# Kernel tuning notes

Measured on AMD Instinct MI355X. Metric: run time of the kernel, lower is better.

## Reference

```python
import jax, jax.numpy as jnp
import numpy as np

T, B, E, H, V, K = 512, 64, 256, 512, 50000, 50
START, STOP = 0, K - 1  # tags = ['<START>'] + tags + ['<STOP>']


def setup_inputs() -> dict:
    key = jax.random.key(0)
    ks = jax.random.split(key, 13)
    p = lambda k, shape, s=0.02: jax.random.normal(k, shape, jnp.float32) * s
    return {
        'tokens': jax.random.randint(ks[0], (T, B), 0, V, dtype=jnp.int32),
        'embed': p(ks[1], (V, E), 0.1),
        'w_ih_f': p(ks[2], (4 * H, E)), 'w_hh_f': p(ks[3], (4 * H, H)), 'b_f': jnp.zeros((4 * H,), jnp.float32),
        'w_ih_b': p(ks[4], (4 * H, E)), 'w_hh_b': p(ks[5], (4 * H, H)), 'b_b': jnp.zeros((4 * H,), jnp.float32),
        'w_enc': p(ks[6], (H, 2 * H)), 'b_enc': jnp.zeros((H,), jnp.float32),
        'w_out': p(ks[7], (K, H)), 'b_out': jnp.zeros((K,), jnp.float32),
        'trans': p(ks[8], (K, K), 0.1),
    }


def _lstm_dir(x, w_ih, w_hh, b, reverse):
    # x: [T,B,E] -> hidden states [T,B,H]; torch gate order i,f,g,o
    bsz = x.shape[1]
    h_dim = w_hh.shape[1]
    xp = jnp.einsum('tbe,ge->tbg', x, w_ih) + b  # precompute input projections

    def step(carry, xt):
        h, c = carry
        g = xt + h @ w_hh.T
        i, f, gg, o = jnp.split(g, 4, axis=-1)
        c = jax.nn.sigmoid(f) * c + jax.nn.sigmoid(i) * jnp.tanh(gg)
        h = jax.nn.sigmoid(o) * jnp.tanh(c)
        return (h, c), h

    init = (jnp.zeros((bsz, h_dim), x.dtype), jnp.zeros((bsz, h_dim), x.dtype))
    _, hs = jax.lax.scan(step, init, xp, reverse=reverse)
    return hs


def reference(tokens, embed, w_ih_f, w_hh_f, b_f, w_ih_b, w_hh_b, b_b,
              w_enc, b_enc, w_out, b_out, trans):
    x = embed[tokens]  # [T,B,E]
    hf = _lstm_dir(x, w_ih_f, w_hh_f, b_f, reverse=False)
    hb = _lstm_dir(x, w_ih_b, w_hh_b, b_b, reverse=True)
    enc = jnp.concatenate([hf, hb], axis=-1)                      # [T,B,2H]
    states = jnp.tanh(jnp.einsum('tbd,hd->tbh', enc, w_enc) + b_enc)
    emit = jnp.einsum('tbh,kh->tbk', states, w_out) + b_out       # [T,B,K]

    # CRF forward algorithm (log partition). trans[j, i] = score of i -> j.
    NEG = jnp.float32(-10000.0)
    bsz, k = emit.shape[1], emit.shape[2]
    alpha0 = jnp.full((bsz, k), NEG).at[:, START].set(0.0)

    def crf_step(alpha, e_t):
        # scores[b, j, i] = alpha[b, i] + trans[j, i] + emit[b, t, j]
        s = alpha[:, None, :] + trans[None, :, :] + e_t[:, :, None]
        return jax.nn.logsumexp(s, axis=-1), None

    alpha, _ = jax.lax.scan(crf_step, alpha0, emit)
    log_z = jax.nn.logsumexp(alpha + trans[STOP][None, :], axis=-1)  # [B]
    return log_z
```

## Files before the change

kernel.cpp:

```cpp
#include <hip/hip_runtime.h>
#include <stdint.h>

#define T_ 512
#define B_ 64
#define E_ 256
#define H_ 512
#define KT 50

typedef __attribute__((ext_vector_type(8))) short bf16x8;
typedef __attribute__((ext_vector_type(4))) float f32x4;
typedef __attribute__((ext_vector_type(4))) int i32x4;

#define MFMA16(a,b,c) __builtin_amdgcn_mfma_f32_16x16x32_bf16((a),(b),(c),0,0,0)

static __device__ __forceinline__ float bf2f(unsigned short v) {
  unsigned int u = ((unsigned int)v) << 16; float f; __builtin_memcpy(&f, &u, 4); return f;
}
static __device__ __forceinline__ unsigned short f2bf(float f) {
  unsigned int u; __builtin_memcpy(&u, &f, 4);
  u += 0x7fffu + ((u >> 16) & 1u);
  return (unsigned short)(u >> 16);
}
static __device__ __forceinline__ float sigm(float x) { return 1.f / (1.f + __expf(-x)); }
static __device__ __forceinline__ float tanh_(float x) { return 2.f / (1.f + __expf(-2.f * x)) - 1.f; }

static __device__ __forceinline__ unsigned int load_dw_dev(const unsigned int* p) {
  unsigned int v;
  asm volatile("global_load_dword %0, %1, off sc0 sc1\n\ts_waitcnt vmcnt(0)"
               : "=v"(v) : "v"(p) : "memory");
  return v;
}

__global__ void probe_kernel(const unsigned short* __restrict__ e,
                             unsigned int* __restrict__ flag) {
  int lane = threadIdx.x & 63;
  float a = fabsf(bf2f(e[2 * lane]));
  int good = (a >= 1e-8f && a <= 4.0f);
  unsigned long long m = __ballot(good);
  if (threadIdx.x == 0) flag[0] = (__popcll(m) >= 48) ? 1u : 0u;
}

struct CvtArgs { const void* src; unsigned short* dst; int n; };
struct CvtPack { CvtArgs a[11]; };

__global__ __launch_bounds__(256) void convert_kernel(CvtPack p,
                                                      const unsigned int* __restrict__ flag) {
  CvtArgs c = p.a[blockIdx.y];
  int i = (blockIdx.x * 256 + threadIdx.x) * 8;
  if (i >= c.n) return;
  int isbf = *flag;
  if (i + 8 <= c.n) {
    if (isbf) {
      *(i32x4*)(c.dst + i) = *(const i32x4*)((const unsigned short*)c.src + i);
    } else {
      const float* s = (const float*)c.src;
      float4 a0 = *(const float4*)(s + i);
      float4 a1 = *(const float4*)(s + i + 4);
      unsigned short o[8] = {f2bf(a0.x), f2bf(a0.y), f2bf(a0.z), f2bf(a0.w),
                             f2bf(a1.x), f2bf(a1.y), f2bf(a1.z), f2bf(a1.w)};
      *(i32x4*)(c.dst + i) = *(i32x4*)o;
    }
  } else {
    for (int j = 0; j < 8; j++) {
      if (i + j < c.n) {
        c.dst[i + j] = isbf ? ((const unsigned short*)c.src)[i + j]
                            : f2bf(((const float*)c.src)[i + j]);
      }
    }
  }
}

__global__ __launch_bounds__(256) void embed_kernel(
    const int* __restrict__ tokens, const void* __restrict__ embed,
    const unsigned int* __restrict__ flag, unsigned short* __restrict__ x) {
  int tid = threadIdx.x;
  int row = blockIdx.x * 8 + (tid >> 5);
  int l = tid & 31;
  int tok = tokens[row];
  if (*flag) {
    const unsigned short* e = (const unsigned short*)embed;
    *(i32x4*)(x + (size_t)row * E_ + l * 8) =
        *(const i32x4*)(e + (size_t)tok * E_ + l * 8);
  } else {
    const float* e = (const float*)embed + (size_t)tok * E_ + l * 8;
    float4 a0 = *(const float4*)e;
    float4 a1 = *(const float4*)(e + 4);
    unsigned short o[8] = {f2bf(a0.x), f2bf(a0.y), f2bf(a0.z), f2bf(a0.w),
                           f2bf(a1.x), f2bf(a1.y), f2bf(a1.z), f2bf(a1.w)};
    *(i32x4*)(x + (size_t)row * E_ + l * 8) = *(i32x4*)o;
  }
}

__global__ __launch_bounds__(256, 1) void lstm_kernel(
    const unsigned short* __restrict__ whh_f, const unsigned short* __restrict__ wih_f,
    const unsigned short* __restrict__ bias_f,
    const unsigned short* __restrict__ whh_b, const unsigned short* __restrict__ wih_b,
    const unsigned short* __restrict__ bias_b,
    const unsigned short* __restrict__ x,
    unsigned short* __restrict__ hf, unsigned short* __restrict__ hb,
    unsigned int* __restrict__ tags) {
  const int tid = threadIdx.x;
  const int wv = tid >> 6, lane = tid & 63, q = lane >> 4, l15 = lane & 15;
  const int bid = blockIdx.x;
  const int dir = bid & 1;
  const int wg = bid >> 1;
  const int u0 = wg * 16;

  const unsigned short* whh = dir ? whh_b : whh_f;
  const unsigned short* wih = dir ? wih_b : wih_f;
  const unsigned short* bvec = dir ? bias_b : bias_f;
  unsigned short* hbuf = dir ? hb : hf;
  unsigned int* tbase = tags + (size_t)dir * 512;

  bf16x8 afrag[4][6];
#pragma unroll
  for (int mt = 0; mt < 4; mt++) {
    int row = mt * H_ + u0 + l15;
#pragma unroll
    for (int kl = 0; kl < 6; kl++) {
      const unsigned short* p = (kl < 4)
          ? (whh + (size_t)row * H_ + (wv * 4 + kl) * 32 + q * 8)
          : (wih + (size_t)row * E_ + (wv * 2 + (kl - 4)) * 32 + q * 8);
      afrag[mt][kl] = *(const bf16x8*)p;
    }
  }

  const int eb = tid & 63;
  const int uu = tid >> 6;
  float bg[4][4];
#pragma unroll
  for (int s = 0; s < 4; s++) {
    int u = uu + 4 * s;
#pragma unroll
    for (int g = 0; g < 4; g++) bg[s][g] = bf2f(bvec[g * H_ + u0 + u]);
  }
  float cst[4] = {0.f, 0.f, 0.f, 0.f};

  __shared__ float pacc[4][64][66];
  __shared__ __align__(16) unsigned short h_out[64][16];
  __shared__ unsigned int go_word;
  if (tid == 0) go_word = 0;

  for (int step = 0; step < T_; step++) {
    const int t = dir ? (T_ - 1 - step) : step;
    f32x4 acc[4][4];
#pragma unroll
    for (int mt = 0; mt < 4; mt++)
#pragma unroll
      for (int nt = 0; nt < 4; nt++) acc[mt][nt] = (f32x4){0.f, 0.f, 0.f, 0.f};

    {
      const unsigned short* xb = x + (size_t)t * B_ * E_;
#pragma unroll
      for (int kl = 4; kl < 6; kl++) {
        int ec = wv * 2 + (kl - 4);
#pragma unroll
        for (int nt = 0; nt < 4; nt++) {
          int b = nt * 16 + l15;
          bf16x8 bx = *(const bf16x8*)(xb + (size_t)b * E_ + ec * 32 + q * 8);
#pragma unroll
          for (int mt = 0; mt < 4; mt++)
            acc[mt][nt] = MFMA16(afrag[mt][kl], bx, acc[mt][nt]);
        }
      }
    }

    if (step > 0) {
      if (wv == 1) {
        const unsigned int* tp = tbase + (size_t)(lane & 31) * 16;
        for (;;) {
          unsigned int v = load_dw_dev(tp);
          unsigned long long m = __ballot((lane < 32) ? (v >= (unsigned)step) : 1);
          if (m == ~0ULL) break;
          __builtin_amdgcn_s_sleep(1);
        }
        __hip_atomic_store(&go_word, (unsigned int)step, __ATOMIC_RELAXED,
                           __HIP_MEMORY_SCOPE_WORKGROUP);
      } else {
        while (__hip_atomic_load(&go_word, __ATOMIC_RELAXED,
                                 __HIP_MEMORY_SCOPE_WORKGROUP) < (unsigned int)step)
          __builtin_amdgcn_s_sleep(1);
      }
      asm volatile("" ::: "memory");

      const int tprev = dir ? (t + 1) : (t - 1);
      const unsigned int* hD = (const unsigned int*)hbuf + (size_t)tprev * 16384;

      const unsigned int* a0 = hD + ((wv * 4 + 0) * 4 + q) * 256 + l15 * 4;
      const unsigned int* a1 = hD + ((wv * 4 + 1) * 4 + q) * 256 + l15 * 4;
      const unsigned int* a2 = hD + ((wv * 4 + 2) * 4 + q) * 256 + l15 * 4;
      const unsigned int* a3 = hD + ((wv * 4 + 3) * 4 + q) * 256 + l15 * 4;
      i32x4 h00, h01, h02, h03, h10, h11, h12, h13;
      i32x4 h20, h21, h22, h23, h30, h31, h32, h33;
      asm volatile(
          "global_load_dwordx4 %0, %16, off sc0 sc1\n\t"
          "global_load_dwordx4 %1, %16, off offset:1024 sc0 sc1\n\t"
          "global_load_dwordx4 %2, %16, off offset:2048 sc0 sc1\n\t"
          "global_load_dwordx4 %3, %16, off offset:3072 sc0 sc1\n\t"
          "global_load_dwordx4 %4, %17, off sc0 sc1\n\t"
          "global_load_dwordx4 %5, %17, off offset:1024 sc0 sc1\n\t"
          "global_load_dwordx4 %6, %17, off offset:2048 sc0 sc1\n\t"
          "global_load_dwordx4 %7, %17, off offset:3072 sc0 sc1\n\t"
          "global_load_dwordx4 %8, %18, off sc0 sc1\n\t"
          "global_load_dwordx4 %9, %18, off offset:1024 sc0 sc1\n\t"
          "global_load_dwordx4 %10, %18, off offset:2048 sc0 sc1\n\t"
          "global_load_dwordx4 %11, %18, off offset:3072 sc0 sc1\n\t"
          "global_load_dwordx4 %12, %19, off sc0 sc1\n\t"
          "global_load_dwordx4 %13, %19, off offset:1024 sc0 sc1\n\t"
          "global_load_dwordx4 %14, %19, off offset:2048 sc0 sc1\n\t"
          "global_load_dwordx4 %15, %19, off offset:3072 sc0 sc1\n\t"
          "s_waitcnt vmcnt(0)"
          : "=&v"(h00), "=&v"(h01), "=&v"(h02), "=&v"(h03),
            "=&v"(h10), "=&v"(h11), "=&v"(h12), "=&v"(h13),
            "=&v"(h20), "=&v"(h21), "=&v"(h22), "=&v"(h23),
            "=&v"(h30), "=&v"(h31), "=&v"(h32), "=&v"(h33)
          : "v"(a0), "v"(a1), "v"(a2), "v"(a3)
          : "memory");
      i32x4 hr4[16] = {h00, h01, h02, h03, h10, h11, h12, h13,
                       h20, h21, h22, h23, h30, h31, h32, h33};
#pragma unroll
      for (int kl = 0; kl < 4; kl++) {
#pragma unroll
        for (int nt = 0; nt < 4; nt++) {
          bf16x8 bh;
          __builtin_memcpy(&bh, &hr4[kl * 4 + nt], 16);
#pragma unroll
          for (int mt = 0; mt < 4; mt++)
            acc[mt][nt] = MFMA16(afrag[mt][kl], bh, acc[mt][nt]);
        }
      }
    }

    __syncthreads();
#pragma unroll
    for (int mt = 0; mt < 4; mt++)
#pragma unroll
      for (int nt = 0; nt < 4; nt++)
#pragma unroll
        for (int r = 0; r < 4; r++)
          pacc[wv][mt * 16 + q * 4 + r][nt * 16 + l15] = acc[mt][nt][r];
    __syncthreads();

#pragma unroll
    for (int s = 0; s < 4; s++) {
      int u = uu + 4 * s;
      float gi = bg[s][0], gf = bg[s][1], gg = bg[s][2], og = bg[s][3];
#pragma unroll
      for (int w = 0; w < 4; w++) {
        gi += pacc[w][u][eb];
        gf += pacc[w][16 + u][eb];
        gg += pacc[w][32 + u][eb];
        og += pacc[w][48 + u][eb];
      }
      float cn = sigm(gf) * cst[s] + sigm(gi) * tanh_(gg);
      cst[s] = cn;
      h_out[eb][u] = f2bf(sigm(og) * tanh_(cn));
    }
    __syncthreads();

    if (wv == 0) {
      unsigned int* gp = (unsigned int*)hbuf + (size_t)t * 16384 + wg * 512 + lane * 4;
      i32x4 v0 = *(const i32x4*)&h_out[lane][0];
      i32x4 v1 = *(const i32x4*)&h_out[lane][8];
      asm volatile(
          "global_store_dwordx4 %0, %1, off sc0 sc1\n\t"
          "global_store_dwordx4 %0, %2, off offset:1024 sc0 sc1\n\t"
          "s_waitcnt vmcnt(0)"
          :: "v"(gp), "v"(v0), "v"(v1) : "memory");
      if (lane == 0) {
        unsigned int* tp = tbase + (size_t)wg * 16;
        unsigned int tv = (unsigned int)(step + 1);
        asm volatile("global_store_dword %0, %1, off sc0 sc1"
                     :: "v"(tp), "v"(tv) : "memory");
      }
    }
  }
}

__global__ __launch_bounds__(256) void enc_kernel(
    const unsigned short* __restrict__ hf, const unsigned short* __restrict__ hb,
    const unsigned short* __restrict__ w_enc, const unsigned short* __restrict__ b_enc,
    unsigned short* __restrict__ states) {
  const int tid = threadIdx.x;
  const int bm = blockIdx.x, bn = blockIdx.y;
  const int wv = tid >> 6, lane = tid & 63, q = lane >> 4, l15 = lane & 15;
  const int wm = wv >> 1, wn = wv & 1;

  __shared__ __align__(16) unsigned short a_lds[128][72];
  __shared__ __align__(16) unsigned short b_lds[128][72];
  __shared__ __align__(16) unsigned short st_lds[128][136];

  f32x4 acc[4][4];
#pragma unroll
  for (int mt = 0; mt < 4; mt++)
#pragma unroll
    for (int nt = 0; nt < 4; nt++) acc[mt][nt] = (f32x4){0.f, 0.f, 0.f, 0.f};

  for (int c = 0; c < 16; c++) {
    const unsigned short* asrc = (c < 8) ? hf : hb;
    int kof = (c & 7) * 64;
#pragma unroll
    for (int p = 0; p < 4; p++) {
      int u_ = tid + p * 256;
      int r = u_ >> 3, wu = u_ & 7;
      int grow = bm * 128 + r;
      *(i32x4*)&a_lds[r][wu * 8] =
          *(const i32x4*)((const unsigned int*)asrc + (size_t)(grow >> 6) * 16384 +
                          (size_t)((kof >> 3) + wu) * 256 + (grow & 63) * 4);
      *(i32x4*)&b_lds[r][wu * 8] =
          *(const i32x4*)(w_enc + (size_t)(bn * 128 + r) * 1024 + c * 64 + wu * 8);
    }
    __syncthreads();
#pragma unroll
    for (int kk = 0; kk < 64; kk += 32) {
      bf16x8 af[4], bfr[4];
#pragma unroll
      for (int mt = 0; mt < 4; mt++)
        af[mt] = *(const bf16x8*)&a_lds[wm * 64 + mt * 16 + l15][kk + q * 8];
#pragma unroll
      for (int nt = 0; nt < 4; nt++)
        bfr[nt] = *(const bf16x8*)&b_lds[wn * 64 + nt * 16 + l15][kk + q * 8];
#pragma unroll
      for (int mt = 0; mt < 4; mt++)
#pragma unroll
        for (int nt = 0; nt < 4; nt++) acc[mt][nt] = MFMA16(af[mt], bfr[nt], acc[mt][nt]);
    }
    __syncthreads();
  }

  float be[4];
#pragma unroll
  for (int nt = 0; nt < 4; nt++)
    be[nt] = bf2f(b_enc[bn * 128 + wn * 64 + nt * 16 + l15]);
#pragma unroll
  for (int mt = 0; mt < 4; mt++)
#pragma unroll
    for (int nt = 0; nt < 4; nt++)
#pragma unroll
      for (int r = 0; r < 4; r++) {
        float v = tanh_(acc[mt][nt][r] + be[nt]);
        st_lds[wm * 64 + mt * 16 + q * 4 + r][wn * 64 + nt * 16 + l15] = f2bf(v);
      }
  __syncthreads();
#pragma unroll
  for (int p = 0; p < 8; p++) {
    int u_ = tid + p * 256;
    int r = u_ >> 4, w = u_ & 15;
    *(i32x4*)(states + (size_t)(bm * 128 + r) * H_ + bn * 128 + w * 8) =
        *(const i32x4*)&st_lds[r][w * 8];
  }
}

__global__ __launch_bounds__(256) void emit_kernel(
    const unsigned short* __restrict__ states, const unsigned short* __restrict__ w_out,
    const unsigned short* __restrict__ b_out, float* __restrict__ emit) {
  const int tid = threadIdx.x;
  const int bm = blockIdx.x;
  const int wv = tid >> 6, lane = tid & 63, q = lane >> 4, l15 = lane & 15;
  const int wm = wv >> 1, wn = wv & 1;

  __shared__ __align__(16) unsigned short wo_lds[64][520];
  __shared__ __align__(16) unsigned short a_lds[128][72];

#pragma unroll
  for (int p = 0; p < 16; p++) {
    int u = tid + p * 256;
    int r = u >> 6, wu = u & 63;
    i32x4 v = {0, 0, 0, 0};
    if (r < KT) v = *(const i32x4*)(w_out + (size_t)r * H_ + wu * 8);
    *(i32x4*)&wo_lds[r][wu * 8] = v;
  }

  f32x4 acc[4][2];
#pragma unroll
  for (int mt = 0; mt < 4; mt++)
#pragma unroll
    for (int nt = 0; nt < 2; nt++) acc[mt][nt] = (f32x4){0.f, 0.f, 0.f, 0.f};

  for (int c = 0; c < 8; c++) {
    __syncthreads();
#pragma unroll
    for (int p = 0; p < 4; p++) {
      int u = tid + p * 256;
      int r = u >> 3, wu = u & 7;
      *(i32x4*)&a_lds[r][wu * 8] =
          *(const i32x4*)(states + (size_t)(bm * 128 + r) * H_ + c * 64 + wu * 8);
    }
    __syncthreads();
#pragma unroll
    for (int kk = 0; kk < 64; kk += 32) {
      bf16x8 af[4], bfr[2];
#pragma unroll
      for (int mt = 0; mt < 4; mt++)
        af[mt] = *(const bf16x8*)&a_lds[wm * 64 + mt * 16 + l15][kk + q * 8];
#pragma unroll
      for (int nt = 0; nt < 2; nt++)
        bfr[nt] = *(const bf16x8*)&wo_lds[wn * 32 + nt * 16 + l15][c * 64 + kk + q * 8];
#pragma unroll
      for (int mt = 0; mt < 4; mt++)
#pragma unroll
        for (int nt = 0; nt < 2; nt++) acc[mt][nt] = MFMA16(af[mt], bfr[nt], acc[mt][nt]);
    }
  }

  float bo[2];
#pragma unroll
  for (int nt = 0; nt < 2; nt++) {
    int n = wn * 32 + nt * 16 + l15;
    bo[nt] = (n < KT) ? bf2f(b_out[n]) : 0.f;
  }
#pragma unroll
  for (int mt = 0; mt < 4; mt++)
#pragma unroll
    for (int nt = 0; nt < 2; nt++) {
      int n = wn * 32 + nt * 16 + l15;
      if (n < KT) {
#pragma unroll
        for (int r = 0; r < 4; r++) {
          int m = bm * 128 + wm * 64 + mt * 16 + q * 4 + r;
          emit[(size_t)m * KT + n] = acc[mt][nt][r] + bo[nt];
        }
      }
    }
}

__global__ __launch_bounds__(256) void crf_kernel(
    const float* __restrict__ emit, const unsigned short* __restrict__ trans,
    const unsigned int* __restrict__ flag, void* __restrict__ out) {
  const int tid = threadIdx.x;
  const int wv = tid >> 6, lane = tid & 63;
  const int b = blockIdx.x * 4 + wv;
  const int jj = (lane < KT) ? lane : (KT - 1);

  float tr[KT];
  float mj = -1e30f;
#pragma unroll
  for (int i = 0; i < KT; i++) {
    tr[i] = bf2f(trans[jj * KT + i]);
    mj = fmaxf(mj, tr[i]);
  }
  float et[KT];
#pragma unroll
  for (int i = 0; i < KT; i++) et[i] = __expf(tr[i] - mj);
  float tr_stop = bf2f(trans[(KT - 1) * KT + jj]);

  float alpha = (lane == 0) ? 0.f : -1e30f;
  float e_next = emit[(size_t)b * KT + jj];

  for (int t = 0; t < T_; t++) {
    float e_cur = e_next;
    if (t < T_ - 1) e_next = emit[((size_t)(t + 1) * B_ + b) * KT + jj];
    float M = alpha;
#pragma unroll
    for (int off = 32; off; off >>= 1) M = fmaxf(M, __shfl_xor(M, off, 64));
    float p = __expf(alpha - M);
    float s = 0.f;
#pragma unroll
    for (int i = 0; i < KT; i++) {
      float pi = __uint_as_float(__builtin_amdgcn_readlane(__float_as_uint(p), i));
      s = __builtin_fmaf(et[i], pi, s);
    }
    float an = e_cur + mj + M + __logf(s);
    alpha = (lane < KT) ? an : -1e30f;
  }

  float v = (lane < KT) ? (alpha + tr_stop) : -1e30f;
  float M2 = v;
#pragma unroll
  for (int off = 32; off; off >>= 1) M2 = fmaxf(M2, __shfl_xor(M2, off, 64));
  float s2 = (lane < KT) ? __expf(v - M2) : 0.f;
#pragma unroll
  for (int off = 32; off; off >>= 1) s2 += __shfl_xor(s2, off, 64);
  float lz = M2 + __logf(s2);
  if (lane == 0) {
    if (*flag) ((unsigned short*)out)[b] = f2bf(lz);
    else ((float*)out)[b] = lz;
  }
}

extern "C" void kernel_launch(void* const* d_in, const int* in_sizes, int n_in,
                              void* d_out, int out_size, void* d_ws, size_t ws_size,
                              hipStream_t stream) {
  const int* tokens = (const int*)d_in[0];
  const void* embed = d_in[1];
  const void* wih_f = d_in[2];
  const void* whh_f = d_in[3];
  const void* b_f = d_in[4];
  const void* wih_b = d_in[5];
  const void* whh_b = d_in[6];
  const void* b_b = d_in[7];
  const void* w_enc = d_in[8];
  const void* b_enc = d_in[9];
  const void* w_out = d_in[10];
  const void* b_out = d_in[11];
  const void* trans = d_in[12];

  char* ws = (char*)d_ws;
  unsigned int* tags = (unsigned int*)ws;
  unsigned int* pflag = (unsigned int*)(ws + 262144);
  unsigned short* xbuf = (unsigned short*)(ws + 262400);
  unsigned short* hf = (unsigned short*)(ws + 17039616);
  unsigned short* hb = (unsigned short*)(ws + 50594048);
  unsigned short* states = (unsigned short*)(ws + 84148480);
  float* emit = (float*)(ws + 117702912);
  unsigned short* canon = (unsigned short*)(ws + 124256512);

  unsigned short* c_wih_f = canon + 0;
  unsigned short* c_whh_f = canon + 524288;
  unsigned short* c_b_f   = canon + 1572864;
  unsigned short* c_wih_b = canon + 1574912;
  unsigned short* c_whh_b = canon + 2099200;
  unsigned short* c_b_b   = canon + 3147776;
  unsigned short* c_w_enc = canon + 3149824;
  unsigned short* c_b_enc = canon + 3674112;
  unsigned short* c_w_out = canon + 3674624;
  unsigned short* c_b_out = canon + 3700224;
  unsigned short* c_trans = canon + 3700352;

  hipMemsetAsync(tags, 0, 4096, stream);
  probe_kernel<<<1, 64, 0, stream>>>((const unsigned short*)embed, pflag);

  CvtPack pk;
  pk.a[0]  = {wih_f, c_wih_f, 524288};
  pk.a[1]  = {whh_f, c_whh_f, 1048576};
  pk.a[2]  = {b_f,   c_b_f,   2048};
  pk.a[3]  = {wih_b, c_wih_b, 524288};
  pk.a[4]  = {whh_b, c_whh_b, 1048576};
  pk.a[5]  = {b_b,   c_b_b,   2048};
  pk.a[6]  = {w_enc, c_w_enc, 524288};
  pk.a[7]  = {b_enc, c_b_enc, 512};
  pk.a[8]  = {w_out, c_w_out, 25600};
  pk.a[9]  = {b_out, c_b_out, 50};
  pk.a[10] = {trans, c_trans, 2500};
  convert_kernel<<<dim3(512, 11), 256, 0, stream>>>(pk, pflag);

  embed_kernel<<<(T_ * B_) / 8, 256, 0, stream>>>(tokens, embed, pflag, xbuf);
  lstm_kernel<<<64, 256, 0, stream>>>(c_whh_f, c_wih_f, c_b_f,
                                      c_whh_b, c_wih_b, c_b_b,
                                      xbuf, hf, hb, tags);
  enc_kernel<<<dim3(256, 4), 256, 0, stream>>>(hf, hb, c_w_enc, c_b_enc, states);
  emit_kernel<<<256, 256, 0, stream>>>(states, c_w_out, c_b_out, emit);
  crf_kernel<<<16, 256, 0, stream>>>(emit, c_trans, pflag, d_out);
}
```

Before: 2.783 ms.

## Replace LSTM flag barrier with poisoned h buffer polling and prefetch x

Drops the per-step tag-counter barrier between LSTM workgroups. The h buffers are now pre-filled with a 0xFFFFFFFF sentinel by a new poison kernel, and consumers reload h chunks until no sentinel values remain. It also prefetches the next timestep's x fragments into registers during the current step and removes the trailing vmcnt waits after stores. This removes one round trip of flag store plus poll per step. The risk is that a genuine bf16 pair equal to 0xFFFF (a NaN pattern) would spin forever. It also adds a 64MB poison write before the LSTM runs.

Result: slower. 4.492 ms (+61.4%).

```diff
diff --git a/kernel.cpp b/kernel.cpp
--- a/kernel.cpp
+++ b/kernel.cpp
@@ -23,13 +23,6 @@
 }
 static __device__ __forceinline__ float sigm(float x) { return 1.f / (1.f + __expf(-x)); }
 static __device__ __forceinline__ float tanh_(float x) { return 2.f / (1.f + __expf(-2.f * x)) - 1.f; }
-
-static __device__ __forceinline__ unsigned int load_dw_dev(const unsigned int* p) {
-  unsigned int v;
-  asm volatile("global_load_dword %0, %1, off sc0 sc1\n\ts_waitcnt vmcnt(0)"
-               : "=v"(v) : "v"(p) : "memory");
-  return v;
-}
 
 __global__ void probe_kernel(const unsigned short* __restrict__ e,
                              unsigned int* __restrict__ flag) {
@@ -91,14 +84,50 @@
   }
 }
 
+__global__ __launch_bounds__(256) void poison_kernel(unsigned int* __restrict__ p) {
+  i32x4 v; v[0] = -1; v[1] = -1; v[2] = -1; v[3] = -1;
+  unsigned int* a = p + (size_t)blockIdx.x * 8192 + (size_t)threadIdx.x * 4;
+#pragma unroll
+  for (int k = 0; k < 8; k++) {
+    asm volatile("global_store_dwordx4 %0, %1, off sc0 sc1" :: "v"(a), "v"(v) : "memory");
+    a += 1024;
+  }
+}
+
+#define ISSUE_BX(tt)                                                          \
+  do {                                                                        \
+    const unsigned short* xb_ = x + (size_t)(tt) * (B_ * E_);                 \
+    const unsigned short* x0_ = xb_ + (size_t)(0 * 16 + l15) * E_ + (wv * 2 + 0) * 32 + q * 8; \
+    const unsigned short* x1_ = xb_ + (size_t)(1 * 16 + l15) * E_ + (wv * 2 + 0) * 32 + q * 8; \
+    const unsigned short* x2_ = xb_ + (size_t)(2 * 16 + l15) * E_ + (wv * 2 + 0) * 32 + q * 8; \
+    const unsigned short* x3_ = xb_ + (size_t)(3 * 16 + l15) * E_ + (wv * 2 + 0) * 32 + q * 8; \
+    const unsigned short* x4_ = xb_ + (size_t)(0 * 16 + l15) * E_ + (wv * 2 + 1) * 32 + q * 8; \
+    const unsigned short* x5_ = xb_ + (size_t)(1 * 16 + l15) * E_ + (wv * 2 + 1) * 32 + q * 8; \
+    const unsigned short* x6_ = xb_ + (size_t)(2 * 16 + l15) * E_ + (wv * 2 + 1) * 32 + q * 8; \
+    const unsigned short* x7_ = xb_ + (size_t)(3 * 16 + l15) * E_ + (wv * 2 + 1) * 32 + q * 8; \
+    asm volatile(                                                             \
+        "global_load_dwordx4 %0, %8, off\n\t"                                 \
+        "global_load_dwordx4 %1, %9, off\n\t"                                 \
+        "global_load_dwordx4 %2, %10, off\n\t"                                \
+        "global_load_dwordx4 %3, %11, off\n\t"                                \
+        "global_load_dwordx4 %4, %12, off\n\t"                                \
+        "global_load_dwordx4 %5, %13, off\n\t"                                \
+        "global_load_dwordx4 %6, %14, off\n\t"                                \
+        "global_load_dwordx4 %7, %15, off"                                    \
+        : "=&v"(bxw[0]), "=&v"(bxw[1]), "=&v"(bxw[2]), "=&v"(bxw[3]),         \
+          "=&v"(bxw[4]), "=&v"(bxw[5]), "=&v"(bxw[6]), "=&v"(bxw[7])          \
+        : "v"(x0_), "v"(x1_), "v"(x2_), "v"(x3_),                             \
+          "v"(x4_), "v"(x5_), "v"(x6_), "v"(x7_)                              \
+        : "memory");                                                          \
+  } while (0)
+
 __global__ __launch_bounds__(256, 1) void lstm_kernel(
     const unsigned short* __restrict__ whh_f, const unsigned short* __restrict__ wih_f,
     const unsigned short* __restrict__ bias_f,
     const unsigned short* __restrict__ whh_b, const unsigned short* __restrict__ wih_b,
     const unsigned short* __restrict__ bias_b,
     const unsigned short* __restrict__ x,
-    unsigned short* __restrict__ hf, unsigned short* __restrict__ hb,
-    unsigned int* __restrict__ tags) {
+    unsigned short* __restrict__ hf, unsigned short* __restrict__ hb) {
   const int tid = threadIdx.x;
   const int wv = tid >> 6, lane = tid & 63, q = lane >> 4, l15 = lane & 15;
   const int bid = blockIdx.x;
@@ -110,7 +139,6 @@
   const unsigned short* wih = dir ? wih_b : wih_f;
   const unsigned short* bvec = dir ? bias_b : bias_f;
   unsigned short* hbuf = dir ? hb : hf;
-  unsigned int* tbase = tags + (size_t)dir * 512;
 
   bf16x8 afrag[4][6];
 #pragma unroll
@@ -138,8 +166,9 @@
 
   __shared__ float pacc[4][64][66];
   __shared__ __align__(16) unsigned short h_out[64][16];
-  __shared__ unsigned int go_word;
-  if (tid == 0) go_word = 0;
+
+  i32x4 bxw[8];
+  ISSUE_BX(dir ? (T_ - 1) : 0);
 
   for (int step = 0; step < T_; step++) {
     const int t = dir ? (T_ - 1 - step) : step;
@@ -149,49 +178,17 @@
 #pragma unroll
       for (int nt = 0; nt < 4; nt++) acc[mt][nt] = (f32x4){0.f, 0.f, 0.f, 0.f};
 
-    {
-      const unsigned short* xb = x + (size_t)t * B_ * E_;
-#pragma unroll
-      for (int kl = 4; kl < 6; kl++) {
-        int ec = wv * 2 + (kl - 4);
-#pragma unroll
-        for (int nt = 0; nt < 4; nt++) {
-          int b = nt * 16 + l15;
-          bf16x8 bx = *(const bf16x8*)(xb + (size_t)b * E_ + ec * 32 + q * 8);
-#pragma unroll
-          for (int mt = 0; mt < 4; mt++)
-            acc[mt][nt] = MFMA16(afrag[mt][kl], bx, acc[mt][nt]);
-        }
-      }
-    }
+    i32x4 hr4[16];
+    const unsigned int* gab[4];
+    const unsigned int* hD = nullptr;
 
     if (step > 0) {
-      if (wv == 1) {
-        const unsigned int* tp = tbase + (size_t)(lane & 31) * 16;
-        for (;;) {
-          unsigned int v = load_dw_dev(tp);
-          unsigned long long m = __ballot((lane < 32) ? (v >= (unsigned)step) : 1);
-          if (m == ~0ULL) break;
-          __builtin_amdgcn_s_sleep(1);
-        }
-        __hip_atomic_store(&go_word, (unsigned int)step, __ATOMIC_RELAXED,
-                           __HIP_MEMORY_SCOPE_WORKGROUP);
-      } else {
-        while (__hip_atomic_load(&go_word, __ATOMIC_RELAXED,
-                                 __HIP_MEMORY_SCOPE_WORKGROUP) < (unsigned int)step)
-          __builtin_amdgcn_s_sleep(1);
-      }
-      asm volatile("" ::: "memory");
-
       const int tprev = dir ? (t + 1) : (t - 1);
-      const unsigned int* hD = (const unsigned int*)hbuf + (size_t)tprev * 16384;
-
-      const unsigned int* a0 = hD + ((wv * 4 + 0) * 4 + q) * 256 + l15 * 4;
-      const unsigned int* a1 = hD + ((wv * 4 + 1) * 4 + q) * 256 + l15 * 4;
-      const unsigned int* a2 = hD + ((wv * 4 + 2) * 4 + q) * 256 + l15 * 4;
-      const unsigned int* a3 = hD + ((wv * 4 + 3) * 4 + q) * 256 + l15 * 4;
-      i32x4 h00, h01, h02, h03, h10, h11, h12, h13;
-      i32x4 h20, h21, h22, h23, h30, h31, h32, h33;
+      hD = (const unsigned int*)hbuf + (size_t)tprev * 16384;
+      gab[0] = hD + ((wv * 4 + 0) * 4 + q) * 256 + l15 * 4;
+      gab[1] = hD + ((wv * 4 + 1) * 4 + q) * 256 + l15 * 4;
+      gab[2] = hD + ((wv * 4 + 2) * 4 + q) * 256 + l15 * 4;
+      gab[3] = hD + ((wv * 4 + 3) * 4 + q) * 256 + l15 * 4;
       asm volatile(
           "global_load_dwordx4 %0, %16, off sc0 sc1\n\t"
           "global_load_dwordx4 %1, %16, off offset:1024 sc0 sc1\n\t"
@@ -208,16 +205,80 @@
           "global_load_dwordx4 %12, %19, off sc0 sc1\n\t"
           "global_load_dwordx4 %13, %19, off offset:1024 sc0 sc1\n\t"
           "global_load_dwordx4 %14, %19, off offset:2048 sc0 sc1\n\t"
-          "global_load_dwordx4 %15, %19, off offset:3072 sc0 sc1\n\t"
-          "s_waitcnt vmcnt(0)"
-          : "=&v"(h00), "=&v"(h01), "=&v"(h02), "=&v"(h03),
-            "=&v"(h10), "=&v"(h11), "=&v"(h12), "=&v"(h13),
-            "=&v"(h20), "=&v"(h21), "=&v"(h22), "=&v"(h23),
-            "=&v"(h30), "=&v"(h31), "=&v"(h32), "=&v"(h33)
-          : "v"(a0), "v"(a1), "v"(a2), "v"(a3)
+          "global_load_dwordx4 %15, %19, off offset:3072 sc0 sc1"
+          : "=&v"(hr4[0]), "=&v"(hr4[1]), "=&v"(hr4[2]), "=&v"(hr4[3]),
+            "=&v"(hr4[4]), "=&v"(hr4[5]), "=&v"(hr4[6]), "=&v"(hr4[7]),
+            "=&v"(hr4[8]), "=&v"(hr4[9]), "=&v"(hr4[10]), "=&v"(hr4[11]),
+            "=&v"(hr4[12]), "=&v"(hr4[13]), "=&v"(hr4[14]), "=&v"(hr4[15])
+          : "v"(gab[0]), "v"(gab[1]), "v"(gab[2]), "v"(gab[3])
           : "memory");
-      i32x4 hr4[16] = {h00, h01, h02, h03, h10, h11, h12, h13,
-                       h20, h21, h22, h23, h30, h31, h32, h33};
+    }
+
+    if (step == 0) {
+      asm volatile("s_waitcnt vmcnt(0)" ::: "memory");
+    } else {
+      asm volatile("s_waitcnt vmcnt(16)" ::: "memory");
+    }
+    __builtin_amdgcn_sched_barrier(0);
+
+#pragma unroll
+    for (int kl = 0; kl < 2; kl++) {
+#pragma unroll
+      for (int nt = 0; nt < 4; nt++) {
+        bf16x8 b_;
+        __builtin_memcpy(&b_, &bxw[kl * 4 + nt], 16);
+#pragma unroll
+        for (int mt = 0; mt < 4; mt++)
+          acc[mt][nt] = MFMA16(afrag[mt][4 + kl], b_, acc[mt][nt]);
+      }
+    }
+
+    if (step > 0) {
+      __builtin_amdgcn_sched_barrier(0);
+
+      unsigned int vmask = 0;
+#pragma unroll
+      for (int c = 0; c < 16; c++) {
+        const unsigned int* ap = gab[c >> 2] + (c & 3) * 256;
+        int oob = (ap < hD) | ((ap + 4) > (hD + 16384));
+        if (__ballot(oob) == 0ULL) vmask |= (1u << c);
+      }
+
+      for (;;) {
+        asm volatile("s_waitcnt vmcnt(0)" ::: "memory");
+        __builtin_amdgcn_sched_barrier(0);
+        unsigned int pend = 0;
+#pragma unroll
+        for (int c = 0; c < 16; c++) {
+          int bad = (hr4[c][0] == -1) | (hr4[c][1] == -1) |
+                    (hr4[c][2] == -1) | (hr4[c][3] == -1);
+          if (__ballot(bad) != 0ULL) pend |= (1u << c);
+        }
+        pend &= vmask;
+        if (!pend) break;
+#pragma unroll
+        for (int c = 0; c < 16; c++) {
+          if (pend & (1u << c)) {
+            asm volatile("global_load_dwordx4 %0, %1, off sc0 sc1"
+                         : "=&v"(hr4[c])
+                         : "v"(gab[c >> 2] + (c & 3) * 256)
+                         : "memory");
+          }
+        }
+      }
+
+      unsigned int inval = (~vmask) & 0xFFFFu;
+      if (inval) {
+#pragma unroll
+        for (int c = 0; c < 16; c++) {
+          if (inval & (1u << c)) {
+#pragma unroll
+            for (int j = 0; j < 4; j++)
+              hr4[c][j] = (hr4[c][j] == -1) ? 0 : hr4[c][j];
+          }
+        }
+      }
+
 #pragma unroll
       for (int kl = 0; kl < 4; kl++) {
 #pragma unroll
@@ -240,6 +301,8 @@
         for (int r = 0; r < 4; r++)
           pacc[wv][mt * 16 + q * 4 + r][nt * 16 + l15] = acc[mt][nt][r];
     __syncthreads();
+
+    if (step < T_ - 1) ISSUE_BX(dir ? (T_ - 2 - step) : (step + 1));
 
 #pragma unroll
     for (int s = 0; s < 4; s++) {
@@ -264,15 +327,8 @@
       i32x4 v1 = *(const i32x4*)&h_out[lane][8];
       asm volatile(
           "global_store_dwordx4 %0, %1, off sc0 sc1\n\t"
-          "global_store_dwordx4 %0, %2, off offset:1024 sc0 sc1\n\t"
-          "s_waitcnt vmcnt(0)"
+          "global_store_dwordx4 %0, %2, off offset:1024 sc0 sc1"
           :: "v"(gp), "v"(v0), "v"(v1) : "memory");
-      if (lane == 0) {
-        unsigned int* tp = tbase + (size_t)wg * 16;
-        unsigned int tv = (unsigned int)(step + 1);
-        asm volatile("global_store_dword %0, %1, off sc0 sc1"
-                     :: "v"(tp), "v"(tv) : "memory");
-      }
     }
   }
 }
@@ -496,7 +552,6 @@
   const void* trans = d_in[12];
 
   char* ws = (char*)d_ws;
-  unsigned int* tags = (unsigned int*)ws;
   unsigned int* pflag = (unsigned int*)(ws + 262144);
   unsigned short* xbuf = (unsigned short*)(ws + 262400);
   unsigned short* hf = (unsigned short*)(ws + 17039616);
@@ -517,7 +572,6 @@
   unsigned short* c_b_out = canon + 3700224;
   unsigned short* c_trans = canon + 3700352;
 
-  hipMemsetAsync(tags, 0, 4096, stream);
   probe_kernel<<<1, 64, 0, stream>>>((const unsigned short*)embed, pflag);
 
   CvtPack pk;
@@ -535,9 +589,10 @@
   convert_kernel<<<dim3(512, 11), 256, 0, stream>>>(pk, pflag);
 
   embed_kernel<<<(T_ * B_) / 8, 256, 0, stream>>>(tokens, embed, pflag, xbuf);
+  poison_kernel<<<2048, 256, 0, stream>>>((unsigned int*)(ws + 17039616));
   lstm_kernel<<<64, 256, 0, stream>>>(c_whh_f, c_wih_f, c_b_f,
                                       c_whh_b, c_wih_b, c_b_b,
-                                      xbuf, hf, hb, tags);
+                                      xbuf, hf, hb);
   enc_kernel<<<dim3(256, 4), 256, 0, stream>>>(hf, hb, c_w_enc, c_b_enc, states);
   emit_kernel<<<256, 256, 0, stream>>>(states, c_w_out, c_b_out, emit);
   crf_kernel<<<16, 256, 0, stream>>>(emit, c_trans, pflag, d_out);
```

## Prefetch next-step x tiles and poll tag flags from every wave

Applied to the files above, without the earlier changes.

The x-projection operands for the next timestep are now loaded into registers during the current step, so that load latency overlaps with the gate computation. The input MFMAs are issued while the h loads are still in flight. The LDS go_word handoff is removed: each wave now polls the cross-workgroup tag flags itself, which takes the intra-block broadcast off the critical path. The cost is more register pressure, hand-managed vmcnt waits that depend on the order of outstanding loads, and more global polling traffic.

Result: slower. 2.892 ms (+3.9%).

```diff
diff --git a/kernel.cpp b/kernel.cpp
--- a/kernel.cpp
+++ b/kernel.cpp
@@ -91,6 +91,33 @@
   }
 }
 
+#define ISSUE_BX(tt)                                                          \
+  do {                                                                        \
+    const unsigned short* xb_ = x + (size_t)(tt) * (B_ * E_);                 \
+    const unsigned short* x0_ = xb_ + (size_t)(0 * 16 + l15) * E_ + (wv * 2 + 0) * 32 + q * 8; \
+    const unsigned short* x1_ = xb_ + (size_t)(1 * 16 + l15) * E_ + (wv * 2 + 0) * 32 + q * 8; \
+    const unsigned short* x2_ = xb_ + (size_t)(2 * 16 + l15) * E_ + (wv * 2 + 0) * 32 + q * 8; \
+    const unsigned short* x3_ = xb_ + (size_t)(3 * 16 + l15) * E_ + (wv * 2 + 0) * 32 + q * 8; \
+    const unsigned short* x4_ = xb_ + (size_t)(0 * 16 + l15) * E_ + (wv * 2 + 1) * 32 + q * 8; \
+    const unsigned short* x5_ = xb_ + (size_t)(1 * 16 + l15) * E_ + (wv * 2 + 1) * 32 + q * 8; \
+    const unsigned short* x6_ = xb_ + (size_t)(2 * 16 + l15) * E_ + (wv * 2 + 1) * 32 + q * 8; \
+    const unsigned short* x7_ = xb_ + (size_t)(3 * 16 + l15) * E_ + (wv * 2 + 1) * 32 + q * 8; \
+    asm volatile(                                                             \
+        "global_load_dwordx4 %0, %8, off\n\t"                                 \
+        "global_load_dwordx4 %1, %9, off\n\t"                                 \
+        "global_load_dwordx4 %2, %10, off\n\t"                                \
+        "global_load_dwordx4 %3, %11, off\n\t"                                \
+        "global_load_dwordx4 %4, %12, off\n\t"                                \
+        "global_load_dwordx4 %5, %13, off\n\t"                                \
+        "global_load_dwordx4 %6, %14, off\n\t"                                \
+        "global_load_dwordx4 %7, %15, off"                                    \
+        : "=&v"(bxw[0]), "=&v"(bxw[1]), "=&v"(bxw[2]), "=&v"(bxw[3]),         \
+          "=&v"(bxw[4]), "=&v"(bxw[5]), "=&v"(bxw[6]), "=&v"(bxw[7])          \
+        : "v"(x0_), "v"(x1_), "v"(x2_), "v"(x3_),                             \
+          "v"(x4_), "v"(x5_), "v"(x6_), "v"(x7_)                              \
+        : "memory");                                                          \
+  } while (0)
+
 __global__ __launch_bounds__(256, 1) void lstm_kernel(
     const unsigned short* __restrict__ whh_f, const unsigned short* __restrict__ wih_f,
     const unsigned short* __restrict__ bias_f,
@@ -125,6 +152,11 @@
     }
   }
 
+  int poff = (l15 < 10) ? l15 : 0;
+  int pidx = wv * 8 + poff;
+  if (pidx > 31) pidx = 31;
+  const unsigned int* my_tp = tbase + (size_t)pidx * 16;
+
   const int eb = tid & 63;
   const int uu = tid >> 6;
   float bg[4][4];
@@ -138,8 +170,9 @@
 
   __shared__ float pacc[4][64][66];
   __shared__ __align__(16) unsigned short h_out[64][16];
-  __shared__ unsigned int go_word;
-  if (tid == 0) go_word = 0;
+
+  i32x4 bxw[8];
+  ISSUE_BX(dir ? (T_ - 1) : 0);
 
   for (int step = 0; step < T_; step++) {
     const int t = dir ? (T_ - 1 - step) : step;
@@ -149,49 +182,30 @@
 #pragma unroll
       for (int nt = 0; nt < 4; nt++) acc[mt][nt] = (f32x4){0.f, 0.f, 0.f, 0.f};
 
-    {
-      const unsigned short* xb = x + (size_t)t * B_ * E_;
-#pragma unroll
-      for (int kl = 4; kl < 6; kl++) {
-        int ec = wv * 2 + (kl - 4);
-#pragma unroll
-        for (int nt = 0; nt < 4; nt++) {
-          int b = nt * 16 + l15;
-          bf16x8 bx = *(const bf16x8*)(xb + (size_t)b * E_ + ec * 32 + q * 8);
-#pragma unroll
-          for (int mt = 0; mt < 4; mt++)
-            acc[mt][nt] = MFMA16(afrag[mt][kl], bx, acc[mt][nt]);
-        }
-      }
-    }
-
+    if (step == 0) {
+      asm volatile("s_waitcnt vmcnt(0)" ::: "memory");
+    } else if (wv == 0) {
+      asm volatile("s_waitcnt vmcnt(1)" ::: "memory");
+    } else {
+      asm volatile("s_waitcnt vmcnt(0)" ::: "memory");
+    }
+    __builtin_amdgcn_sched_barrier(0);
+
+    i32x4 hr4[16];
     if (step > 0) {
-      if (wv == 1) {
-        const unsigned int* tp = tbase + (size_t)(lane & 31) * 16;
-        for (;;) {
-          unsigned int v = load_dw_dev(tp);
-          unsigned long long m = __ballot((lane < 32) ? (v >= (unsigned)step) : 1);
-          if (m == ~0ULL) break;
-          __builtin_amdgcn_s_sleep(1);
-        }
-        __hip_atomic_store(&go_word, (unsigned int)step, __ATOMIC_RELAXED,
-                           __HIP_MEMORY_SCOPE_WORKGROUP);
-      } else {
-        while (__hip_atomic_load(&go_word, __ATOMIC_RELAXED,
-                                 __HIP_MEMORY_SCOPE_WORKGROUP) < (unsigned int)step)
-          __builtin_amdgcn_s_sleep(1);
+      for (;;) {
+        unsigned int v = load_dw_dev(my_tp);
+        if (__ballot(v >= (unsigned)step) == ~0ULL) break;
+        __builtin_amdgcn_s_sleep(1);
       }
       asm volatile("" ::: "memory");
 
       const int tprev = dir ? (t + 1) : (t - 1);
       const unsigned int* hD = (const unsigned int*)hbuf + (size_t)tprev * 16384;
-
       const unsigned int* a0 = hD + ((wv * 4 + 0) * 4 + q) * 256 + l15 * 4;
       const unsigned int* a1 = hD + ((wv * 4 + 1) * 4 + q) * 256 + l15 * 4;
       const unsigned int* a2 = hD + ((wv * 4 + 2) * 4 + q) * 256 + l15 * 4;
       const unsigned int* a3 = hD + ((wv * 4 + 3) * 4 + q) * 256 + l15 * 4;
-      i32x4 h00, h01, h02, h03, h10, h11, h12, h13;
-      i32x4 h20, h21, h22, h23, h30, h31, h32, h33;
       asm volatile(
           "global_load_dwordx4 %0, %16, off sc0 sc1\n\t"
           "global_load_dwordx4 %1, %16, off offset:1024 sc0 sc1\n\t"
@@ -208,16 +222,31 @@
           "global_load_dwordx4 %12, %19, off sc0 sc1\n\t"
           "global_load_dwordx4 %13, %19, off offset:1024 sc0 sc1\n\t"
           "global_load_dwordx4 %14, %19, off offset:2048 sc0 sc1\n\t"
-          "global_load_dwordx4 %15, %19, off offset:3072 sc0 sc1\n\t"
-          "s_waitcnt vmcnt(0)"
-          : "=&v"(h00), "=&v"(h01), "=&v"(h02), "=&v"(h03),
-            "=&v"(h10), "=&v"(h11), "=&v"(h12), "=&v"(h13),
-            "=&v"(h20), "=&v"(h21), "=&v"(h22), "=&v"(h23),
-            "=&v"(h30), "=&v"(h31), "=&v"(h32), "=&v"(h33)
+          "global_load_dwordx4 %15, %19, off offset:3072 sc0 sc1"
+          : "=&v"(hr4[0]), "=&v"(hr4[1]), "=&v"(hr4[2]), "=&v"(hr4[3]),
+            "=&v"(hr4[4]), "=&v"(hr4[5]), "=&v"(hr4[6]), "=&v"(hr4[7]),
+            "=&v"(hr4[8]), "=&v"(hr4[9]), "=&v"(hr4[10]), "=&v"(hr4[11]),
+            "=&v"(hr4[12]), "=&v"(hr4[13]), "=&v"(hr4[14]), "=&v"(hr4[15])
           : "v"(a0), "v"(a1), "v"(a2), "v"(a3)
           : "memory");
-      i32x4 hr4[16] = {h00, h01, h02, h03, h10, h11, h12, h13,
-                       h20, h21, h22, h23, h30, h31, h32, h33};
+    }
+
+#pragma unroll
+    for (int kl = 0; kl < 2; kl++) {
+#pragma unroll
+      for (int nt = 0; nt < 4; nt++) {
+        bf16x8 b_;
+        __builtin_memcpy(&b_, &bxw[kl * 4 + nt], 16);
+#pragma unroll
+        for (int mt = 0; mt < 4; mt++)
+          acc[mt][nt] = MFMA16(afrag[mt][4 + kl], b_, acc[mt][nt]);
+      }
+    }
+
+    if (step > 0) {
+      asm volatile("s_waitcnt vmcnt(0)" ::: "memory");
+      __builtin_amdgcn_sched_barrier(0);
+
 #pragma unroll
       for (int kl = 0; kl < 4; kl++) {
 #pragma unroll
@@ -240,6 +269,8 @@
         for (int r = 0; r < 4; r++)
           pacc[wv][mt * 16 + q * 4 + r][nt * 16 + l15] = acc[mt][nt][r];
     __syncthreads();
+
+    if (step < T_ - 1) ISSUE_BX(dir ? (T_ - 2 - step) : (step + 1));
 
 #pragma unroll
     for (int s = 0; s < 4; s++) {
```
